# Performance work log

Hardware: AMD Instinct MI355X
Metric: run time of the kernel (lower is better)

The kernel has to match this reference:

```python
import math
import jax, jax.numpy as jnp
import numpy as np

B, L, D, H = 256, 32, 512, 512
NEG_INF = -1e9


def setup_inputs() -> dict:
    key = jax.random.key(0)
    ks = jax.random.split(key, 7)
    x = jax.random.normal(ks[0], (B, L, D), dtype=jnp.float32)
    length = jax.random.randint(ks[1], (B,), 2, L + 1)  # valid lengths in [2, L]
    # word_linear: D -> 2H
    W_word = jax.random.normal(ks[2], (2 * H, D), dtype=jnp.float32) * (1.0 / math.sqrt(D))
    b_word = jnp.zeros((2 * H,), dtype=jnp.float32)
    # comp_linear: 2H -> 5H (orthogonal-ish init; scale is fine for a reference)
    W_comp = jax.random.normal(ks[3], (5 * H, 2 * H), dtype=jnp.float32) * (1.0 / math.sqrt(2 * H))
    b_comp = jnp.zeros((5 * H,), dtype=jnp.float32)
    comp_query = jax.random.normal(ks[4], (H,), dtype=jnp.float32) * 0.01
    return {"x": x, "length": length, "W_word": W_word, "b_word": b_word,
            "W_comp": W_comp, "b_comp": b_comp, "comp_query": comp_query}


def _treelstm_compose(hl, cl, hr, cr, W_comp, b_comp):
    # hl/hr: [B, n, H] -> parent h, c: [B, n, H]
    v = jnp.einsum('bnd,kd->bnk', jnp.concatenate([hl, hr], axis=2), W_comp) + b_comp
    i, fl, fr, u, o = jnp.split(v, 5, axis=2)
    c = cl * jax.nn.sigmoid(fl + 1.0) + cr * jax.nn.sigmoid(fr + 1.0) \
        + jnp.tanh(u) * jax.nn.sigmoid(i)
    h = jax.nn.sigmoid(o) * jnp.tanh(c)
    return h, c


def reference(x, length, W_word, b_word, W_comp, b_comp, comp_query):
    length_mask = (jnp.arange(L)[None, :] < length[:, None]).astype(jnp.float32)  # [B, L]
    # leaf states from word_linear (use_leaf_rnn=False path)
    hc = jnp.einsum('bld,kd->blk', x, W_word) + b_word  # [B, L, 2H]
    h, c = jnp.split(hc, 2, axis=2)
    scale = 1.0 / math.sqrt(H)
    for i in range(L - 1):
        new_h, new_c = _treelstm_compose(h[:, :-1], c[:, :-1], h[:, 1:], c[:, 1:], W_comp, b_comp)
        if i < L - 2:
            # eval-mode greedy composition selection (basic.greedy_select)
            logits = jnp.sum(comp_query * new_h, axis=-1) * scale  # [B, L-1-i]
            mask = length_mask[:, i + 1:]
            logits = jnp.where(mask > 0, logits, NEG_INF)
            select = jax.nn.one_hot(jnp.argmax(logits, axis=1), logits.shape[1], dtype=jnp.float32)
            cum = jnp.cumsum(select, axis=1)
            left = (1.0 - cum)[:, :, None]
            right = (cum - select)[:, :, None]
            sel = select[:, :, None]
            new_h = sel * new_h + left * h[:, :-1] + right * h[:, 1:]
            new_c = sel * new_c + left * c[:, :-1] + right * c[:, 1:]
        done = length_mask[:, i + 1][:, None, None]
        h = done * new_h + (1.0 - done) * h[:, :-1]
        c = done * new_c + (1.0 - done) * c[:, :-1]
    return h[:, 0, :]  # final root hidden state [B, H]
```

## Files before the change

### kernel.cpp

```cpp
#include <hip/hip_runtime.h>
#include <cmath>

#define B_   256
#define L_   32
#define H_   512
#define NH5  2560
#define N2   5120
#define SCALE 0.044194173824159216f

__device__ float g_h [B_*L_*H_];
__device__ float g_c [B_*L_*H_];
__device__ float g_al[(size_t)B_*L_*NH5];
__device__ float g_ar[(size_t)B_*L_*NH5];
__device__ float g_logit[B_*L_];
__device__ int   g_list[B_*L_];
__device__ int   g_count[B_];
__device__ int   g_merged[B_];
__device__ int   g_mpos[B_];
__device__ int   g_off[B_];
__device__ int   g_rows[B_*L_];
__device__ int   g_nrows;
__device__ int   g_mlist[2][B_];
__device__ int   g_cnt[2];

__device__ __forceinline__ float sigm(float x) { return 1.0f / (1.0f + expf(-x)); }

__global__ __launch_bounds__(256) void init_all(const int* __restrict__ length) {
  __shared__ int sw[4];
  const int t = threadIdx.x;
  const int len = length[t];
  int v = len;
#pragma unroll
  for (int off = 1; off < 64; off <<= 1) {
    int o = __shfl_up(v, off, 64);
    if ((t & 63) >= off) v += o;
  }
  if ((t & 63) == 63) sw[t >> 6] = v;
  __syncthreads();
  int base = 0;
  for (int w = 0; w < (t >> 6); w++) base += sw[w];
  const int incl = base + v;
  const int off0 = incl - len;
  g_off[t] = off0;
  if (t == 255) g_nrows = incl;
  g_count[t] = len; g_merged[t] = -2; g_mpos[t] = 0;
  if (t == 0) { g_cnt[0] = 0; g_cnt[1] = 0; }
#pragma unroll
  for (int s = 0; s < L_; s++) g_list[t*L_ + s] = s;
  for (int s = 0; s < len; s++) g_rows[off0 + s] = t*L_ + s;
}

template<int MODE>
__global__ __launch_bounds__(256) void gemm_big(
    const float* __restrict__ Aext,
    const float* __restrict__ Bm,
    const float* __restrict__ bias)
{
  const int NR = g_nrows;
  const int m0 = blockIdx.y * 128;
  if (m0 >= NR) return;
  const int n0 = blockIdx.x * 128;

  const int tid = threadIdx.x;
  const int w = tid >> 6, l = tid & 63;
  const int tx = (w & 1) * 8 + (l & 7);
  const int ty = (w >> 1) * 8 + (l >> 3);

  __shared__ float As[8][128];
  __shared__ float Bs[8][128];

  const int ra = tid >> 1, qa = (tid & 1) * 4;

  const float* Abase = (MODE == 0) ? Aext : g_h;
  int mr = m0 + ra; if (mr >= NR) mr = NR - 1;
  const float* aptr = Abase + (size_t)g_rows[mr] * 512 + qa;

  const float* bptr;
  {
    int nrow = n0 + ra;
    if (MODE == 0) bptr = Bm + (size_t)nrow * 512 + qa;
    else bptr = Bm + (nrow < NH5 ? (size_t)nrow * 1024
                                 : (size_t)(nrow - NH5) * 1024 + 512) + qa;
  }

  float4 av = *(const float4*)(aptr);
  float4 bv = *(const float4*)(bptr);
  float acc[8][8] = {};

  for (int k0 = 0; k0 < 512; k0 += 8) {
    __syncthreads();
    As[qa+0][ra] = av.x; As[qa+1][ra] = av.y; As[qa+2][ra] = av.z; As[qa+3][ra] = av.w;
    Bs[qa+0][ra] = bv.x; Bs[qa+1][ra] = bv.y; Bs[qa+2][ra] = bv.z; Bs[qa+3][ra] = bv.w;
    __syncthreads();
    if (k0 + 8 < 512) {
      av = *(const float4*)(aptr + k0 + 8);
      bv = *(const float4*)(bptr + k0 + 8);
    }
#pragma unroll
    for (int k = 0; k < 8; k++) {
      float af[8], bf[8];
#pragma unroll
      for (int c = 0; c < 2; c++) {
        float4 t = *(const float4*)&As[k][ty*8 + 4*c];
        af[4*c+0]=t.x; af[4*c+1]=t.y; af[4*c+2]=t.z; af[4*c+3]=t.w;
      }
#pragma unroll
      for (int c = 0; c < 2; c++) {
        float4 t = *(const float4*)&Bs[k][tx*8 + 4*c];
        bf[4*c+0]=t.x; bf[4*c+1]=t.y; bf[4*c+2]=t.z; bf[4*c+3]=t.w;
      }
#pragma unroll
      for (int i = 0; i < 8; i++)
#pragma unroll
        for (int j = 0; j < 8; j++)
          acc[i][j] = fmaf(af[i], bf[j], acc[i][j]);
    }
  }

  const int nb = n0 + tx*8;
  float4 bias_lo, bias_hi;
  if (MODE == 0) { bias_lo = *(const float4*)(bias + nb);
                   bias_hi = *(const float4*)(bias + nb + 4); }
#pragma unroll
  for (int i = 0; i < 8; i++) {
    int mrow = m0 + ty*8 + i;
    if (mrow >= NR) continue;
    int crow = g_rows[mrow];
    float4 v0 = make_float4(acc[i][0], acc[i][1], acc[i][2], acc[i][3]);
    float4 v1 = make_float4(acc[i][4], acc[i][5], acc[i][6], acc[i][7]);
    if (MODE == 0) {
      v0.x += bias_lo.x; v0.y += bias_lo.y; v0.z += bias_lo.z; v0.w += bias_lo.w;
      v1.x += bias_hi.x; v1.y += bias_hi.y; v1.z += bias_hi.z; v1.w += bias_hi.w;
      float* dst = (nb < H_) ? g_h + (size_t)crow*H_ + nb
                             : g_c + (size_t)crow*H_ + (nb - H_);
      *(float4*)(dst) = v0; *(float4*)(dst + 4) = v1;
    } else {
      float* dst = (nb < NH5) ? g_al + (size_t)crow*NH5 + nb
                              : g_ar + (size_t)crow*NH5 + (nb - NH5);
      *(float4*)(dst) = v0; *(float4*)(dst + 4) = v1;
    }
  }
}

__global__ __launch_bounds__(256) void iter0_logits(const int* __restrict__ length,
                                                    const float* __restrict__ bc,
                                                    const float* __restrict__ qv) {
  __shared__ float sred[4];
  const int p = blockIdx.x, b = blockIdx.y;
  if (p >= length[b] - 1) return;
  const float* al = g_al + (size_t)(b*L_ + p)*NH5;
  const float* ar = g_ar + (size_t)(b*L_ + p + 1)*NH5;
  const float* cl = g_c  + (size_t)(b*L_ + p)*H_;
  const float* cr = g_c  + (size_t)(b*L_ + p + 1)*H_;
  float part = 0.f;
#pragma unroll
  for (int jj = 0; jj < H_/256; jj++) {
    int j = threadIdx.x + jj*256;
    float vi  = al[j]       + ar[j]       + bc[j];
    float vfl = al[H_+j]    + ar[H_+j]    + bc[H_+j];
    float vfr = al[2*H_+j]  + ar[2*H_+j]  + bc[2*H_+j];
    float vu  = al[3*H_+j]  + ar[3*H_+j]  + bc[3*H_+j];
    float vo  = al[4*H_+j]  + ar[4*H_+j]  + bc[4*H_+j];
    float c = cl[j]*sigm(vfl+1.f) + cr[j]*sigm(vfr+1.f) + tanhf(vu)*sigm(vi);
    float h = sigm(vo)*tanhf(c);
    part = fmaf(qv[j], h, part);
  }
#pragma unroll
  for (int off = 32; off; off >>= 1) part += __shfl_down(part, off, 64);
  if ((threadIdx.x & 63) == 0) sred[threadIdx.x >> 6] = part;
  __syncthreads();
  if (threadIdx.x == 0)
    g_logit[b*L_ + p] = (sred[0]+sred[1]+sred[2]+sred[3]) * SCALE;
}

__global__ __launch_bounds__(256) void select_merge(int iter,
    const int* __restrict__ length,
    const float* __restrict__ bc,
    const float* __restrict__ qv,
    float* __restrict__ out)
{
  __shared__ float sred[4];
  __shared__ int s_sel[3];
  const int b = blockIdx.x, tid = threadIdx.x;
  if (b == 0 && tid == 0) g_cnt[(iter & 1) ^ 1] = 0;

  const int m     = g_count[b];
  const int pslot = g_merged[b];
  const int ppos  = g_mpos[b];
  int* list = g_list + b*L_;

  if (iter > 0 && pslot >= 0) {
    const int half = tid >> 7, lt = tid & 127;
    int sl = -1, sr = -1;
    if (half == 0) { if (ppos > 0)     { sl = list[ppos-1]; sr = list[ppos];   } }
    else           { if (ppos < m - 1) { sl = list[ppos];   sr = list[ppos+1]; } }
    float part = 0.f;
    if (sl >= 0) {
      const float* al = g_al + (size_t)(b*L_+sl)*NH5;
      const float* ar = g_ar + (size_t)(b*L_+sr)*NH5;
      const float* cl = g_c  + (size_t)(b*L_+sl)*H_;
      const float* cr = g_c  + (size_t)(b*L_+sr)*H_;
      const int j = lt * 4;
      float4 ai  = *(const float4*)(al + j)        , bi  = *(const float4*)(ar + j);
      float4 afl = *(const float4*)(al + H_   + j) , bfl = *(const float4*)(ar + H_   + j);
      float4 afr = *(const float4*)(al + 2*H_ + j) , bfr = *(const float4*)(ar + 2*H_ + j);
      float4 au  = *(const float4*)(al + 3*H_ + j) , bu  = *(const float4*)(ar + 3*H_ + j);
      float4 ao  = *(const float4*)(al + 4*H_ + j) , bo  = *(const float4*)(ar + 4*H_ + j);
      float4 c4l = *(const float4*)(cl + j)        , c4r = *(const float4*)(cr + j);
      float4 q4  = *(const float4*)(qv + j);
      const float* bc0 = bc + j;
      float c, h;
      c = c4l.x*sigm(afl.x+bfl.x+bc0[H_]+1.f)   + c4r.x*sigm(afr.x+bfr.x+bc0[2*H_]+1.f)
        + tanhf(au.x+bu.x+bc0[3*H_])*sigm(ai.x+bi.x+bc0[0]);
      h = sigm(ao.x+bo.x+bc0[4*H_])*tanhf(c);   part = fmaf(q4.x, h, part);
      c = c4l.y*sigm(afl.y+bfl.y+bc0[H_+1]+1.f) + c4r.y*sigm(afr.y+bfr.y+bc0[2*H_+1]+1.f)
        + tanhf(au.y+bu.y+bc0[3*H_+1])*sigm(ai.y+bi.y+bc0[1]);
      h = sigm(ao.y+bo.y+bc0[4*H_+1])*tanhf(c); part = fmaf(q4.y, h, part);
      c = c4l.z*sigm(afl.z+bfl.z+bc0[H_+2]+1.f) + c4r.z*sigm(afr.z+bfr.z+bc0[2*H_+2]+1.f)
        + tanhf(au.z+bu.z+bc0[3*H_+2])*sigm(ai.z+bi.z+bc0[2]);
      h = sigm(ao.z+bo.z+bc0[4*H_+2])*tanhf(c); part = fmaf(q4.z, h, part);
      c = c4l.w*sigm(afl.w+bfl.w+bc0[H_+3]+1.f) + c4r.w*sigm(afr.w+bfr.w+bc0[2*H_+3]+1.f)
        + tanhf(au.w+bu.w+bc0[3*H_+3])*sigm(ai.w+bi.w+bc0[3]);
      h = sigm(ao.w+bo.w+bc0[4*H_+3])*tanhf(c); part = fmaf(q4.w, h, part);
    }
#pragma unroll
    for (int off = 32; off; off >>= 1) part += __shfl_down(part, off, 64);
    if ((tid & 63) == 0) sred[tid >> 6] = part;
    __syncthreads();
    if (tid == 0   && ppos > 0)     g_logit[b*L_ + list[ppos-1]] = (sred[0]+sred[1])*SCALE;
    if (tid == 128 && ppos < m - 1) g_logit[b*L_ + list[ppos]]   = (sred[2]+sred[3])*SCALE;
  }

  const bool active = iter < (length[b] - 1);
  if (active) {
    __syncthreads();

    if (tid < 64) {
      float lg = -1e30f; int idx = tid;
      if (tid < m - 1) lg = g_logit[b*L_ + list[tid]];
#pragma unroll
      for (int off = 32; off; off >>= 1) {
        float olg = __shfl_down(lg, off, 64);
        int   oid = __shfl_down(idx, off, 64);
        if (olg > lg || (olg == lg && oid < idx)) { lg = olg; idx = oid; }
      }
      if (tid == 0) { s_sel[0] = idx; s_sel[1] = list[idx]; s_sel[2] = list[idx+1]; }
    }
    __syncthreads();
    const int pos = s_sel[0], sl = s_sel[1], sr = s_sel[2];

    if (tid < 128) {
      const float* al = g_al + (size_t)(b*L_+sl)*NH5;
      const float* ar = g_ar + (size_t)(b*L_+sr)*NH5;
      float*       cl = g_c  + (size_t)(b*L_+sl)*H_;
      const float* cr = g_c  + (size_t)(b*L_+sr)*H_;
      float*       hl = g_h  + (size_t)(b*L_+sl)*H_;
      const int j = tid * 4;
      float4 ai  = *(const float4*)(al + j)        , bi  = *(const float4*)(ar + j);
      float4 afl = *(const float4*)(al + H_   + j) , bfl = *(const float4*)(ar + H_   + j);
      float4 afr = *(const float4*)(al + 2*H_ + j) , bfr = *(const float4*)(ar + 2*H_ + j);
      float4 au  = *(const float4*)(al + 3*H_ + j) , bu  = *(const float4*)(ar + 3*H_ + j);
      float4 ao  = *(const float4*)(al + 4*H_ + j) , bo  = *(const float4*)(ar + 4*H_ + j);
      float4 c4l = *(const float4*)(cl + j)        , c4r = *(const float4*)(cr + j);
      const float* bc0 = bc + j;
      float4 cn, hn;
      cn.x = c4l.x*sigm(afl.x+bfl.x+bc0[H_]+1.f)   + c4r.x*sigm(afr.x+bfr.x+bc0[2*H_]+1.f)
           + tanhf(au.x+bu.x+bc0[3*H_])*sigm(ai.x+bi.x+bc0[0]);
      hn.x = sigm(ao.x+bo.x+bc0[4*H_])*tanhf(cn.x);
      cn.y = c4l.y*sigm(afl.y+bfl.y+bc0[H_+1]+1.f) + c4r.y*sigm(afr.y+bfr.y+bc0[2*H_+1]+1.f)
           + tanhf(au.y+bu.y+bc0[3*H_+1])*sigm(ai.y+bi.y+bc0[1]);
      hn.y = sigm(ao.y+bo.y+bc0[4*H_+1])*tanhf(cn.y);
      cn.z = c4l.z*sigm(afl.z+bfl.z+bc0[H_+2]+1.f) + c4r.z*sigm(afr.z+bfr.z+bc0[2*H_+2]+1.f)
           + tanhf(au.z+bu.z+bc0[3*H_+2])*sigm(ai.z+bi.z+bc0[2]);
      hn.z = sigm(ao.z+bo.z+bc0[4*H_+2])*tanhf(cn.z);
      cn.w = c4l.w*sigm(afl.w+bfl.w+bc0[H_+3]+1.f) + c4r.w*sigm(afr.w+bfr.w+bc0[2*H_+3]+1.f)
           + tanhf(au.w+bu.w+bc0[3*H_+3])*sigm(ai.w+bi.w+bc0[3]);
      hn.w = sigm(ao.w+bo.w+bc0[4*H_+3])*tanhf(cn.w);
      *(float4*)(cl + j) = cn;
      *(float4*)(hl + j) = hn;
    }
    __syncthreads();
    if (tid == 0) {
      for (int n = pos+1; n < m-1; n++) list[n] = list[n+1];
      g_count[b]  = m - 1;
      g_merged[b] = sl;
      g_mpos[b]   = pos;
      int k = atomicAdd(&g_cnt[iter & 1], 1);
      g_mlist[iter & 1][k] = b;
    }
  } else {
    if (tid == 0) g_merged[b] = -1;
  }

  if (iter == L_-2) {
    __syncthreads();
    for (int j = tid; j < H_; j += 256)
      out[(size_t)b*H_ + j] = g_h[(size_t)(b*L_)*H_ + j];
  }
}

__global__ __launch_bounds__(256) void gemm_iter(int par, const float* __restrict__ Wc)
{
  const int nact = g_cnt[par];
  const int m0 = blockIdx.y * 32;
  if (m0 >= nact) return;
  const int n0 = blockIdx.x * 64;
  const int tid = threadIdx.x;

  __shared__ float As[32][32];
  __shared__ float Bs[32][64];

  const int ra = tid >> 3, qa = (tid & 7) * 4;
  int mr = m0 + ra; if (mr >= nact) mr = nact - 1;
  const int bbA = g_mlist[par][mr];
  const float* aptr = g_h + (size_t)(bbA*L_ + g_merged[bbA]) * 512 + qa;

  const int rb = tid >> 2, qb = (tid & 3) * 8;
  const int nr = n0 + rb;
  const float* bptr = (nr < NH5) ? Wc + (size_t)nr * 1024 + qb
                                 : Wc + (size_t)(nr - NH5) * 1024 + 512 + qb;

  const int tx = tid & 15, ty = tid >> 4;

  float4 av  = *(const float4*)(aptr);
  float4 bv0 = *(const float4*)(bptr);
  float4 bv1 = *(const float4*)(bptr + 4);
  float acc[2][4] = {};

  for (int k0 = 0; k0 < 512; k0 += 32) {
    __syncthreads();
    As[qa+0][ra] = av.x;  As[qa+1][ra] = av.y;  As[qa+2][ra] = av.z;  As[qa+3][ra] = av.w;
    Bs[qb+0][rb] = bv0.x; Bs[qb+1][rb] = bv0.y; Bs[qb+2][rb] = bv0.z; Bs[qb+3][rb] = bv0.w;
    Bs[qb+4][rb] = bv1.x; Bs[qb+5][rb] = bv1.y; Bs[qb+6][rb] = bv1.z; Bs[qb+7][rb] = bv1.w;
    __syncthreads();
    if (k0 + 32 < 512) {
      av  = *(const float4*)(aptr + k0 + 32);
      bv0 = *(const float4*)(bptr + k0 + 32);
      bv1 = *(const float4*)(bptr + k0 + 36);
    }
#pragma unroll
    for (int k = 0; k < 32; k++) {
      float2 a2 = *(const float2*)&As[k][ty*2];
      float4 b4 = *(const float4*)&Bs[k][tx*4];
      acc[0][0] = fmaf(a2.x, b4.x, acc[0][0]);
      acc[0][1] = fmaf(a2.x, b4.y, acc[0][1]);
      acc[0][2] = fmaf(a2.x, b4.z, acc[0][2]);
      acc[0][3] = fmaf(a2.x, b4.w, acc[0][3]);
      acc[1][0] = fmaf(a2.y, b4.x, acc[1][0]);
      acc[1][1] = fmaf(a2.y, b4.y, acc[1][1]);
      acc[1][2] = fmaf(a2.y, b4.z, acc[1][2]);
      acc[1][3] = fmaf(a2.y, b4.w, acc[1][3]);
    }
  }

#pragma unroll
  for (int i = 0; i < 2; i++) {
    int mrow = m0 + ty*2 + i;
    if (mrow >= nact) continue;
    int bb = g_mlist[par][mrow];
    size_t base = (size_t)(bb*L_ + g_merged[bb]) * NH5;
    int n = n0 + tx*4;
    float4 v = make_float4(acc[i][0], acc[i][1], acc[i][2], acc[i][3]);
    if (n < NH5) *(float4*)(g_al + base + n)         = v;
    else         *(float4*)(g_ar + base + (n - NH5)) = v;
  }
}

extern "C" void kernel_launch(void* const* d_in, const int* in_sizes, int n_in,
                              void* d_out, int out_size, void* d_ws, size_t ws_size,
                              hipStream_t stream)
{
  (void)in_sizes; (void)n_in; (void)out_size; (void)d_ws; (void)ws_size;
  const float* x      = (const float*)d_in[0];
  const int*   length = (const int*)  d_in[1];
  const float* W_word = (const float*)d_in[2];
  const float* b_word = (const float*)d_in[3];
  const float* W_comp = (const float*)d_in[4];
  const float* b_comp = (const float*)d_in[5];
  const float* q      = (const float*)d_in[6];
  float* out = (float*)d_out;

  init_all<<<1, 256, 0, stream>>>(length);

  gemm_big<0><<<dim3(1024/128, 64), 256, 0, stream>>>(x, W_word, b_word);
  gemm_big<1><<<dim3(N2/128,   64), 256, 0, stream>>>(nullptr, W_comp, nullptr);

  iter0_logits<<<dim3(L_-1, B_), 256, 0, stream>>>(length, b_comp, q);

  for (int i = 0; i < L_-1; i++) {
    select_merge<<<B_, 256, 0, stream>>>(i, length, b_comp, q, out);
    if (i < L_-2)
      gemm_iter<<<dim3(N2/64, 8), 256, 0, stream>>>(i & 1, W_comp);
  }
}
```

Baseline: 1.686 ms.

## Use split-bf16 three-limb MFMA for the leaf composition GEMM

Replaces the FP32 SIMT leaf GEMM (h × W_comp, N=5120) with a bf16 MFMA GEMM. Each float is split into three bf16 limbs, and six limb cross-products are accumulated to keep near-FP32 accuracy. A new kernel converts W_comp into limb layout, and the word GEMM epilogue now also writes h as limbs. This trades extra conversion traffic, extra memory and six MFMA passes for matrix-core throughput on the largest one-off GEMM, while the per-iteration gemm_iter stays unchanged.

```diff
diff --git a/kernel.cpp b/kernel.cpp
--- a/kernel.cpp
+++ b/kernel.cpp
@@ -7,6 +7,12 @@
 #define NH5  2560
 #define N2   5120
 #define SCALE 0.044194173824159216f
+
+typedef short bf16x8 __attribute__((ext_vector_type(8)));
+typedef float f32x4  __attribute__((ext_vector_type(4)));
+
+#define HSZ (8192ull*512ull)
+#define WSZ (5120ull*512ull)
 
 __device__ float g_h [B_*L_*H_];
 __device__ float g_c [B_*L_*H_];
@@ -22,8 +28,19 @@
 __device__ int   g_nrows;
 __device__ int   g_mlist[2][B_];
 __device__ int   g_cnt[2];
+__device__ unsigned short g_hL[3*HSZ];
+__device__ unsigned short g_wL[3*WSZ];
 
 __device__ __forceinline__ float sigm(float x) { return 1.0f / (1.0f + expf(-x)); }
+
+__device__ __forceinline__ void limb3(float f, unsigned short& a,
+                                      unsigned short& b, unsigned short& c) {
+  unsigned u0 = __float_as_uint(f); a = (unsigned short)(u0 >> 16);
+  float r1 = f - __uint_as_float(u0 & 0xffff0000u);
+  unsigned u1 = __float_as_uint(r1); b = (unsigned short)(u1 >> 16);
+  float r2 = r1 - __uint_as_float(u1 & 0xffff0000u);
+  c = (unsigned short)(__float_as_uint(r2) >> 16);
+}
 
 __global__ __launch_bounds__(256) void init_all(const int* __restrict__ length) {
   __shared__ int sw[4];
@@ -50,8 +67,22 @@
   for (int s = 0; s < len; s++) g_rows[off0 + s] = t*L_ + s;
 }
 
-template<int MODE>
-__global__ __launch_bounds__(256) void gemm_big(
+__global__ __launch_bounds__(128) void convert_w(const float* __restrict__ Wc) {
+  const int n = blockIdx.x;
+  const float* src = (n < NH5) ? Wc + (size_t)n * 1024
+                               : Wc + (size_t)(n - NH5) * 1024 + 512;
+  const int k = threadIdx.x * 4;
+  float4 f = *(const float4*)(src + k);
+  ushort4 u0, u1, u2;
+  limb3(f.x, u0.x, u1.x, u2.x); limb3(f.y, u0.y, u1.y, u2.y);
+  limb3(f.z, u0.z, u1.z, u2.z); limb3(f.w, u0.w, u1.w, u2.w);
+  const size_t base = (size_t)n * 512 + k;
+  *(ushort4*)(g_wL + 0*WSZ + base) = u0;
+  *(ushort4*)(g_wL + 1*WSZ + base) = u1;
+  *(ushort4*)(g_wL + 2*WSZ + base) = u2;
+}
+
+__global__ __launch_bounds__(256) void gemm_word(
     const float* __restrict__ Aext,
     const float* __restrict__ Bm,
     const float* __restrict__ bias)
@@ -71,17 +102,9 @@
 
   const int ra = tid >> 1, qa = (tid & 1) * 4;
 
-  const float* Abase = (MODE == 0) ? Aext : g_h;
   int mr = m0 + ra; if (mr >= NR) mr = NR - 1;
-  const float* aptr = Abase + (size_t)g_rows[mr] * 512 + qa;
-
-  const float* bptr;
-  {
-    int nrow = n0 + ra;
-    if (MODE == 0) bptr = Bm + (size_t)nrow * 512 + qa;
-    else bptr = Bm + (nrow < NH5 ? (size_t)nrow * 1024
-                                 : (size_t)(nrow - NH5) * 1024 + 512) + qa;
-  }
+  const float* aptr = Aext + (size_t)g_rows[mr] * 512 + qa;
+  const float* bptr = Bm + (size_t)(n0 + ra) * 512 + qa;
 
   float4 av = *(const float4*)(aptr);
   float4 bv = *(const float4*)(bptr);
@@ -118,28 +141,138 @@
   }
 
   const int nb = n0 + tx*8;
-  float4 bias_lo, bias_hi;
-  if (MODE == 0) { bias_lo = *(const float4*)(bias + nb);
-                   bias_hi = *(const float4*)(bias + nb + 4); }
+  float4 bias_lo = *(const float4*)(bias + nb);
+  float4 bias_hi = *(const float4*)(bias + nb + 4);
 #pragma unroll
   for (int i = 0; i < 8; i++) {
     int mrow = m0 + ty*8 + i;
     if (mrow >= NR) continue;
     int crow = g_rows[mrow];
-    float4 v0 = make_float4(acc[i][0], acc[i][1], acc[i][2], acc[i][3]);
-    float4 v1 = make_float4(acc[i][4], acc[i][5], acc[i][6], acc[i][7]);
-    if (MODE == 0) {
-      v0.x += bias_lo.x; v0.y += bias_lo.y; v0.z += bias_lo.z; v0.w += bias_lo.w;
-      v1.x += bias_hi.x; v1.y += bias_hi.y; v1.z += bias_hi.z; v1.w += bias_hi.w;
-      float* dst = (nb < H_) ? g_h + (size_t)crow*H_ + nb
-                             : g_c + (size_t)crow*H_ + (nb - H_);
+    float4 v0 = make_float4(acc[i][0]+bias_lo.x, acc[i][1]+bias_lo.y,
+                            acc[i][2]+bias_lo.z, acc[i][3]+bias_lo.w);
+    float4 v1 = make_float4(acc[i][4]+bias_hi.x, acc[i][5]+bias_hi.y,
+                            acc[i][6]+bias_hi.z, acc[i][7]+bias_hi.w);
+    if (nb < H_) {
+      float* dst = g_h + (size_t)crow*H_ + nb;
       *(float4*)(dst) = v0; *(float4*)(dst + 4) = v1;
+      ushort4 a0,a1,a2,b0,b1,b2;
+      limb3(v0.x,a0.x,a1.x,a2.x); limb3(v0.y,a0.y,a1.y,a2.y);
+      limb3(v0.z,a0.z,a1.z,a2.z); limb3(v0.w,a0.w,a1.w,a2.w);
+      limb3(v1.x,b0.x,b1.x,b2.x); limb3(v1.y,b0.y,b1.y,b2.y);
+      limb3(v1.z,b0.z,b1.z,b2.z); limb3(v1.w,b0.w,b1.w,b2.w);
+      const size_t hb = (size_t)crow*512 + nb;
+      *(ushort4*)(g_hL + 0*HSZ + hb) = a0; *(ushort4*)(g_hL + 0*HSZ + hb + 4) = b0;
+      *(ushort4*)(g_hL + 1*HSZ + hb) = a1; *(ushort4*)(g_hL + 1*HSZ + hb + 4) = b1;
+      *(ushort4*)(g_hL + 2*HSZ + hb) = a2; *(ushort4*)(g_hL + 2*HSZ + hb + 4) = b2;
     } else {
-      float* dst = (nb < NH5) ? g_al + (size_t)crow*NH5 + nb
-                              : g_ar + (size_t)crow*NH5 + (nb - NH5);
+      float* dst = g_c + (size_t)crow*H_ + (nb - H_);
       *(float4*)(dst) = v0; *(float4*)(dst + 4) = v1;
     }
   }
+}
+
+__global__ __launch_bounds__(256) void gemm_leaf(void)
+{
+  const int NR = g_nrows;
+  const int m0 = blockIdx.y * 128;
+  if (m0 >= NR) return;
+  const int n0 = blockIdx.x * 128;
+  const int tid = threadIdx.x;
+
+  __shared__ unsigned short As[3][128][40];
+  __shared__ unsigned short Bs[3][128][40];
+  __shared__ int s_rows[128];
+
+  if (tid < 128) {
+    int mr = m0 + tid; if (mr >= NR) mr = NR - 1;
+    s_rows[tid] = g_rows[mr];
+  }
+  __syncthreads();
+
+  const int4* sp[3];
+  int4* lw[3];
+#pragma unroll
+  for (int j = 0; j < 3; j++) {
+    int S = tid + j*256;
+    if (S < 384) {
+      int la = S >> 7, r = S & 127;
+      sp[j] = (const int4*)(g_hL + (size_t)la*HSZ + (size_t)s_rows[r]*512);
+      lw[j] = (int4*)&As[la][r][0];
+    } else {
+      S -= 384;
+      int la = S >> 7, r = S & 127;
+      sp[j] = (const int4*)(g_wL + (size_t)la*WSZ + (size_t)(n0 + r)*512);
+      lw[j] = (int4*)&Bs[la][r][0];
+    }
+  }
+
+  const int lane = tid & 63, w = tid >> 6;
+  const int wm = w >> 1, wn = w & 1;
+  const int lr = lane & 15, qd = lane >> 4;
+
+  f32x4 acc[4][4];
+#pragma unroll
+  for (int i = 0; i < 4; i++)
+#pragma unroll
+    for (int j = 0; j < 4; j++) acc[i][j] = (f32x4){0.f,0.f,0.f,0.f};
+
+  int4 pf[3][4];
+#pragma unroll
+  for (int j = 0; j < 3; j++)
+#pragma unroll
+    for (int q = 0; q < 4; q++) pf[j][q] = sp[j][q];
+
+  for (int ch = 0; ch < 16; ++ch) {
+    __syncthreads();
+#pragma unroll
+    for (int j = 0; j < 3; j++)
+#pragma unroll
+      for (int q = 0; q < 4; q++) lw[j][q] = pf[j][q];
+    __syncthreads();
+    if (ch < 15) {
+#pragma unroll
+      for (int j = 0; j < 3; j++)
+#pragma unroll
+        for (int q = 0; q < 4; q++) pf[j][q] = sp[j][(ch+1)*4 + q];
+    }
+
+    bf16x8 af[3][4];
+#pragma unroll
+    for (int la = 0; la < 3; la++)
+#pragma unroll
+      for (int mt = 0; mt < 4; mt++)
+        af[la][mt] = *(const bf16x8*)&As[la][wm*64 + mt*16 + lr][qd*8];
+
+#pragma unroll
+    for (int lb = 0; lb < 3; lb++) {
+      bf16x8 bf[4];
+#pragma unroll
+      for (int nt = 0; nt < 4; nt++)
+        bf[nt] = *(const bf16x8*)&Bs[lb][wn*64 + nt*16 + lr][qd*8];
+      const int nla = (lb == 0) ? 3 : ((lb == 1) ? 2 : 1);
+      for (int la = 0; la < nla; la++)
+#pragma unroll
+        for (int mt = 0; mt < 4; mt++)
+#pragma unroll
+          for (int nt = 0; nt < 4; nt++)
+            acc[mt][nt] = __builtin_amdgcn_mfma_f32_16x16x32_bf16(
+                af[la][mt], bf[nt], acc[mt][nt], 0, 0, 0);
+    }
+  }
+
+#pragma unroll
+  for (int mt = 0; mt < 4; mt++)
+#pragma unroll
+    for (int nt = 0; nt < 4; nt++) {
+      const int n = n0 + wn*64 + nt*16 + lr;
+      float* dst = (n < NH5) ? g_al + n : g_ar + (n - NH5);
+#pragma unroll
+      for (int r = 0; r < 4; r++) {
+        const int ml = wm*64 + mt*16 + qd*4 + r;
+        if (m0 + ml >= NR) continue;
+        dst[(size_t)s_rows[ml] * NH5] = acc[mt][nt][r];
+      }
+    }
 }
 
 __global__ __launch_bounds__(256) void iter0_logits(const int* __restrict__ length,
@@ -381,9 +514,10 @@
   float* out = (float*)d_out;
 
   init_all<<<1, 256, 0, stream>>>(length);
-
-  gemm_big<0><<<dim3(1024/128, 64), 256, 0, stream>>>(x, W_word, b_word);
-  gemm_big<1><<<dim3(N2/128,   64), 256, 0, stream>>>(nullptr, W_comp, nullptr);
+  convert_w<<<N2, 128, 0, stream>>>(W_comp);
+
+  gemm_word<<<dim3(1024/128, 64), 256, 0, stream>>>(x, W_word, b_word);
+  gemm_leaf<<<dim3(N2/128, 64), 256, 0, stream>>>();
 
   iter0_logits<<<dim3(L_-1, B_), 256, 0, stream>>>(length, b_comp, q);
 
```

Result: slower. 1.868 ms (+10.8%).
